# Kernel tuning notes

Hardware: AMD Instinct MI355X
Metric: run time of the kernel (lower is better)

Reference implementation:

```python
import jax, jax.numpy as jnp
import numpy as np


def setup_inputs() -> dict:
    key = jax.random.key(0)
    k1, k2 = jax.random.split(key)
    b, s, h = 32, 4096, 1024
    decoder_state_t = jax.random.normal(k1, (b, h), dtype=jnp.float32)
    encoder_outputs = jax.random.normal(k2, (b, s, h), dtype=jnp.float32)
    return {"decoder_state_t": decoder_state_t, "encoder_outputs": encoder_outputs}


def reference(decoder_state_t, encoder_outputs):
    # scores[b,s] = sum_h decoder_state_t[b,h] * encoder_outputs[b,s,h]
    scores = jnp.einsum("bh,bsh->bs", decoder_state_t, encoder_outputs)
    attn = jax.nn.softmax(scores, axis=-1)
    # context[b,h] = sum_s attn[b,s] * encoder_outputs[b,s,h]
    context = jnp.einsum("bs,bsh->bh", attn, encoder_outputs)
    return (context, attn)
```

## Files before the change

### kernel.cpp

```cpp
#include <hip/hip_runtime.h>
#include <math.h>

#define B 32
#define S 4096
#define H 1024
#define NCHUNK 32
#define ROWS_PER_BLOCK (S / NCHUNK)
#define ROWS_PER_WAVE (ROWS_PER_BLOCK/4)
#define PSTRIDE 1040

__global__ __launch_bounds__(256) void attn_pass1(
    const float* __restrict__ dec, const float* __restrict__ enc,
    float* __restrict__ scores, float* __restrict__ part)
{
    const int blk   = blockIdx.x;
    const int b     = blk / NCHUNK;
    const int chunk = blk % NCHUNK;
    const int lane  = threadIdx.x & 63;
    const int w     = threadIdx.x >> 6;

    const float4* dsp = (const float4*)(dec + (size_t)b * H);
    const float4 ds0 = dsp[lane];
    const float4 ds1 = dsp[lane + 64];
    const float4 ds2 = dsp[lane + 128];
    const float4 ds3 = dsp[lane + 192];

    float m = -INFINITY, l = 0.f;
    float4 a0 = {0.f,0.f,0.f,0.f}, a1 = a0, a2 = a0, a3 = a0;

    const int row0 = chunk * ROWS_PER_BLOCK + w * ROWS_PER_WAVE;
    for (int r = 0; r < ROWS_PER_WAVE; ++r) {
        const int row = row0 + r;
        const float4* ep = (const float4*)(enc + ((size_t)b * S + row) * H);
        const float4 e0 = ep[lane];
        const float4 e1 = ep[lane + 64];
        const float4 e2 = ep[lane + 128];
        const float4 e3 = ep[lane + 192];

        float p = 0.f;
        p = fmaf(e0.x, ds0.x, p); p = fmaf(e0.y, ds0.y, p);
        p = fmaf(e0.z, ds0.z, p); p = fmaf(e0.w, ds0.w, p);
        p = fmaf(e1.x, ds1.x, p); p = fmaf(e1.y, ds1.y, p);
        p = fmaf(e1.z, ds1.z, p); p = fmaf(e1.w, ds1.w, p);
        p = fmaf(e2.x, ds2.x, p); p = fmaf(e2.y, ds2.y, p);
        p = fmaf(e2.z, ds2.z, p); p = fmaf(e2.w, ds2.w, p);
        p = fmaf(e3.x, ds3.x, p); p = fmaf(e3.y, ds3.y, p);
        p = fmaf(e3.z, ds3.z, p); p = fmaf(e3.w, ds3.w, p);

        p += __shfl_xor(p, 32);
        p += __shfl_xor(p, 16);
        p += __shfl_xor(p, 8);
        p += __shfl_xor(p, 4);
        p += __shfl_xor(p, 2);
        p += __shfl_xor(p, 1);
        const float score = p;

        if (lane == 0) scores[(size_t)b * S + row] = score;

        if (score > m) {
            const float alpha = __expf(m - score);
            m = score;
            l = fmaf(l, alpha, 1.f);
            a0.x = fmaf(a0.x, alpha, e0.x); a0.y = fmaf(a0.y, alpha, e0.y);
            a0.z = fmaf(a0.z, alpha, e0.z); a0.w = fmaf(a0.w, alpha, e0.w);
            a1.x = fmaf(a1.x, alpha, e1.x); a1.y = fmaf(a1.y, alpha, e1.y);
            a1.z = fmaf(a1.z, alpha, e1.z); a1.w = fmaf(a1.w, alpha, e1.w);
            a2.x = fmaf(a2.x, alpha, e2.x); a2.y = fmaf(a2.y, alpha, e2.y);
            a2.z = fmaf(a2.z, alpha, e2.z); a2.w = fmaf(a2.w, alpha, e2.w);
            a3.x = fmaf(a3.x, alpha, e3.x); a3.y = fmaf(a3.y, alpha, e3.y);
            a3.z = fmaf(a3.z, alpha, e3.z); a3.w = fmaf(a3.w, alpha, e3.w);
        } else {
            const float pe = __expf(score - m);
            l += pe;
            a0.x = fmaf(pe, e0.x, a0.x); a0.y = fmaf(pe, e0.y, a0.y);
            a0.z = fmaf(pe, e0.z, a0.z); a0.w = fmaf(pe, e0.w, a0.w);
            a1.x = fmaf(pe, e1.x, a1.x); a1.y = fmaf(pe, e1.y, a1.y);
            a1.z = fmaf(pe, e1.z, a1.z); a1.w = fmaf(pe, e1.w, a1.w);
            a2.x = fmaf(pe, e2.x, a2.x); a2.y = fmaf(pe, e2.y, a2.y);
            a2.z = fmaf(pe, e2.z, a2.z); a2.w = fmaf(pe, e2.w, a2.w);
            a3.x = fmaf(pe, e3.x, a3.x); a3.y = fmaf(pe, e3.y, a3.y);
            a3.z = fmaf(pe, e3.z, a3.z); a3.w = fmaf(pe, e3.w, a3.w);
        }
    }

    __shared__ float sm[4], sl[4];
    __shared__ float sc[4][1024];
    if (lane == 0) { sm[w] = m; sl[w] = l; }
    *(float4*)&sc[w][lane * 4]       = a0;
    *(float4*)&sc[w][lane * 4 + 256] = a1;
    *(float4*)&sc[w][lane * 4 + 512] = a2;
    *(float4*)&sc[w][lane * 4 + 768] = a3;
    __syncthreads();

    const float M  = fmaxf(fmaxf(sm[0], sm[1]), fmaxf(sm[2], sm[3]));
    const float al0 = __expf(sm[0] - M), al1 = __expf(sm[1] - M);
    const float al2 = __expf(sm[2] - M), al3 = __expf(sm[3] - M);
    const float Lb = sl[0]*al0 + sl[1]*al1 + sl[2]*al2 + sl[3]*al3;

    const int t = threadIdx.x;
    const float4 c0 = *(const float4*)&sc[0][t * 4];
    const float4 c1 = *(const float4*)&sc[1][t * 4];
    const float4 c2 = *(const float4*)&sc[2][t * 4];
    const float4 c3 = *(const float4*)&sc[3][t * 4];
    float4 cp;
    cp.x = c0.x*al0 + c1.x*al1 + c2.x*al2 + c3.x*al3;
    cp.y = c0.y*al0 + c1.y*al1 + c2.y*al2 + c3.y*al3;
    cp.z = c0.z*al0 + c1.z*al1 + c2.z*al2 + c3.z*al3;
    cp.w = c0.w*al0 + c1.w*al1 + c2.w*al2 + c3.w*al3;

    float* pb = part + (size_t)blk * PSTRIDE;
    *(float4*)&pb[t * 4] = cp;
    if (t == 0) { pb[1024] = M; pb[1025] = Lb; }
}

__global__ __launch_bounds__(256) void attn_pass2(
    const float* __restrict__ scores, const float* __restrict__ part,
    float* __restrict__ out)
{
    const int b = blockIdx.x >> 2;
    const int j = blockIdx.x & 3;
    const int t = threadIdx.x;
    const float* pbase = part + (size_t)b * NCHUNK * PSTRIDE;

    float M = -INFINITY;
    for (int i = 0; i < NCHUNK; ++i)
        M = fmaxf(M, pbase[i * PSTRIDE + 1024]);
    float L = 0.f;
    for (int i = 0; i < NCHUNK; ++i)
        L += pbase[i * PSTRIDE + 1025] * __expf(pbase[i * PSTRIDE + 1024] - M);
    const float invL = 1.f / L;

    const int h = j * 256 + t;
    float acc = 0.f;
    for (int i = 0; i < NCHUNK; ++i)
        acc = fmaf(__expf(pbase[i * PSTRIDE + 1024] - M),
                   pbase[i * PSTRIDE + h], acc);
    out[(size_t)b * H + h] = acc * invL;

    float* attn_out = out + (size_t)B * H;
    for (int k = 0; k < 4; ++k) {
        const int s = j * 1024 + k * 256 + t;
        attn_out[(size_t)b * S + s] =
            __expf(scores[(size_t)b * S + s] - M) * invL;
    }
}

extern "C" void kernel_launch(void* const* d_in, const int* in_sizes, int n_in,
                              void* d_out, int out_size, void* d_ws, size_t ws_size,
                              hipStream_t stream) {
    const float* dec = (const float*)d_in[0];
    const float* enc = (const float*)d_in[1];
    float* out = (float*)d_out;
    float* ws  = (float*)d_ws;
    float* scores = ws;
    float* part   = ws + (size_t)B * S;

    attn_pass1<<<B * NCHUNK, 256, 0, stream>>>(dec, enc, scores, part);
    attn_pass2<<<B * 4, 256, 0, stream>>>(scores, part, out);
}
```

Measured before the change: 684.7 us.

## Double-buffer encoder row loads and process two rows per online-softmax step

Rewrites the pass-1 main loop to software-prefetch the next two encoder rows into registers while computing on the current two. Scores for both rows are computed and reduced together, and the online softmax is updated branchlessly, with one rescale per pair of rows. The aim is to hide global memory latency and cut divergent branches and per-row exp/rescale overhead. In exchange it raises register pressure, which may reduce occupancy.

```diff
diff --git a/kernel.cpp b/kernel.cpp
--- a/kernel.cpp
+++ b/kernel.cpp
@@ -8,6 +8,10 @@
 #define ROWS_PER_BLOCK (S / NCHUNK)
 #define ROWS_PER_WAVE (ROWS_PER_BLOCK/4)
 #define PSTRIDE 1040
+
+__device__ __forceinline__ float dot4(float4 a, float4 b) {
+    return fmaf(a.x, b.x, fmaf(a.y, b.y, fmaf(a.z, b.z, a.w * b.w)));
+}
 
 __global__ __launch_bounds__(256) void attn_pass1(
     const float* __restrict__ dec, const float* __restrict__ enc,
@@ -20,76 +24,77 @@
     const int w     = threadIdx.x >> 6;
 
     const float4* dsp = (const float4*)(dec + (size_t)b * H);
-    const float4 ds0 = dsp[lane];
-    const float4 ds1 = dsp[lane + 64];
-    const float4 ds2 = dsp[lane + 128];
-    const float4 ds3 = dsp[lane + 192];
+    float4 dsv[4];
+#pragma unroll
+    for (int q = 0; q < 4; ++q) dsv[q] = dsp[q * 64 + lane];
 
     float m = -INFINITY, l = 0.f;
-    float4 a0 = {0.f,0.f,0.f,0.f}, a1 = a0, a2 = a0, a3 = a0;
+    float4 accq[4];
+#pragma unroll
+    for (int q = 0; q < 4; ++q) accq[q] = make_float4(0.f, 0.f, 0.f, 0.f);
 
     const int row0 = chunk * ROWS_PER_BLOCK + w * ROWS_PER_WAVE;
-    for (int r = 0; r < ROWS_PER_WAVE; ++r) {
-        const int row = row0 + r;
-        const float4* ep = (const float4*)(enc + ((size_t)b * S + row) * H);
-        const float4 e0 = ep[lane];
-        const float4 e1 = ep[lane + 64];
-        const float4 e2 = ep[lane + 128];
-        const float4 e3 = ep[lane + 192];
+    const float4* base = (const float4*)(enc + ((size_t)b * S + row0) * H);
 
-        float p = 0.f;
-        p = fmaf(e0.x, ds0.x, p); p = fmaf(e0.y, ds0.y, p);
-        p = fmaf(e0.z, ds0.z, p); p = fmaf(e0.w, ds0.w, p);
-        p = fmaf(e1.x, ds1.x, p); p = fmaf(e1.y, ds1.y, p);
-        p = fmaf(e1.z, ds1.z, p); p = fmaf(e1.w, ds1.w, p);
-        p = fmaf(e2.x, ds2.x, p); p = fmaf(e2.y, ds2.y, p);
-        p = fmaf(e2.z, ds2.z, p); p = fmaf(e2.w, ds2.w, p);
-        p = fmaf(e3.x, ds3.x, p); p = fmaf(e3.y, ds3.y, p);
-        p = fmaf(e3.z, ds3.z, p); p = fmaf(e3.w, ds3.w, p);
+    float4 buf[2][2][4];
+#pragma unroll
+    for (int q = 0; q < 4; ++q) {
+        buf[0][0][q] = base[q * 64 + lane];
+        buf[0][1][q] = base[256 + q * 64 + lane];
+    }
 
-        p += __shfl_xor(p, 32);
-        p += __shfl_xor(p, 16);
-        p += __shfl_xor(p, 8);
-        p += __shfl_xor(p, 4);
-        p += __shfl_xor(p, 2);
-        p += __shfl_xor(p, 1);
-        const float score = p;
+#pragma unroll
+    for (int rr = 0; rr < ROWS_PER_WAVE; rr += 2) {
+        const int pc = (rr >> 1) & 1;
+        const int pn = pc ^ 1;
+        if (rr + 2 < ROWS_PER_WAVE) {
+            const float4* nb = base + (size_t)(rr + 2) * 256;
+#pragma unroll
+            for (int q = 0; q < 4; ++q) {
+                buf[pn][0][q] = nb[q * 64 + lane];
+                buf[pn][1][q] = nb[256 + q * 64 + lane];
+            }
+        }
 
-        if (lane == 0) scores[(size_t)b * S + row] = score;
+        float s0 = (dot4(buf[pc][0][0], dsv[0]) + dot4(buf[pc][0][1], dsv[1]))
+                 + (dot4(buf[pc][0][2], dsv[2]) + dot4(buf[pc][0][3], dsv[3]));
+        float s1 = (dot4(buf[pc][1][0], dsv[0]) + dot4(buf[pc][1][1], dsv[1]))
+                 + (dot4(buf[pc][1][2], dsv[2]) + dot4(buf[pc][1][3], dsv[3]));
 
-        if (score > m) {
-            const float alpha = __expf(m - score);
-            m = score;
-            l = fmaf(l, alpha, 1.f);
-            a0.x = fmaf(a0.x, alpha, e0.x); a0.y = fmaf(a0.y, alpha, e0.y);
-            a0.z = fmaf(a0.z, alpha, e0.z); a0.w = fmaf(a0.w, alpha, e0.w);
-            a1.x = fmaf(a1.x, alpha, e1.x); a1.y = fmaf(a1.y, alpha, e1.y);
-            a1.z = fmaf(a1.z, alpha, e1.z); a1.w = fmaf(a1.w, alpha, e1.w);
-            a2.x = fmaf(a2.x, alpha, e2.x); a2.y = fmaf(a2.y, alpha, e2.y);
-            a2.z = fmaf(a2.z, alpha, e2.z); a2.w = fmaf(a2.w, alpha, e2.w);
-            a3.x = fmaf(a3.x, alpha, e3.x); a3.y = fmaf(a3.y, alpha, e3.y);
-            a3.z = fmaf(a3.z, alpha, e3.z); a3.w = fmaf(a3.w, alpha, e3.w);
-        } else {
-            const float pe = __expf(score - m);
-            l += pe;
-            a0.x = fmaf(pe, e0.x, a0.x); a0.y = fmaf(pe, e0.y, a0.y);
-            a0.z = fmaf(pe, e0.z, a0.z); a0.w = fmaf(pe, e0.w, a0.w);
-            a1.x = fmaf(pe, e1.x, a1.x); a1.y = fmaf(pe, e1.y, a1.y);
-            a1.z = fmaf(pe, e1.z, a1.z); a1.w = fmaf(pe, e1.w, a1.w);
-            a2.x = fmaf(pe, e2.x, a2.x); a2.y = fmaf(pe, e2.y, a2.y);
-            a2.z = fmaf(pe, e2.z, a2.z); a2.w = fmaf(pe, e2.w, a2.w);
-            a3.x = fmaf(pe, e3.x, a3.x); a3.y = fmaf(pe, e3.y, a3.y);
-            a3.z = fmaf(pe, e3.z, a3.z); a3.w = fmaf(pe, e3.w, a3.w);
+#pragma unroll
+        for (int d = 32; d >= 1; d >>= 1) {
+            s0 += __shfl_xor(s0, d);
+            s1 += __shfl_xor(s1, d);
+        }
+
+        if (lane == 0) {
+            float2 sv = make_float2(s0, s1);
+            *(float2*)&scores[(size_t)b * S + row0 + rr] = sv;
+        }
+
+        const float mn = fmaxf(m, fmaxf(s0, s1));
+        const float a  = __expf(m - mn);
+        const float p0 = __expf(s0 - mn);
+        const float p1 = __expf(s1 - mn);
+        m = mn;
+        l = fmaf(l, a, p0 + p1);
+#pragma unroll
+        for (int q = 0; q < 4; ++q) {
+            const float4 e0 = buf[pc][0][q];
+            const float4 e1 = buf[pc][1][q];
+            accq[q].x = fmaf(p1, e1.x, fmaf(p0, e0.x, accq[q].x * a));
+            accq[q].y = fmaf(p1, e1.y, fmaf(p0, e0.y, accq[q].y * a));
+            accq[q].z = fmaf(p1, e1.z, fmaf(p0, e0.z, accq[q].z * a));
+            accq[q].w = fmaf(p1, e1.w, fmaf(p0, e0.w, accq[q].w * a));
         }
     }
 
     __shared__ float sm[4], sl[4];
     __shared__ float sc[4][1024];
     if (lane == 0) { sm[w] = m; sl[w] = l; }
-    *(float4*)&sc[w][lane * 4]       = a0;
-    *(float4*)&sc[w][lane * 4 + 256] = a1;
-    *(float4*)&sc[w][lane * 4 + 512] = a2;
-    *(float4*)&sc[w][lane * 4 + 768] = a3;
+#pragma unroll
+    for (int q = 0; q < 4; ++q)
+        *(float4*)&sc[w][(q * 64 + lane) * 4] = accq[q];
     __syncthreads();
 
     const float M  = fmaxf(fmaxf(sm[0], sm[1]), fmaxf(sm[2], sm[3]));
```

New measurement: 757.7 us. 10.7% more time.
